# Performance work log

Hardware: AMD Instinct MI355X
Metric: run time of the kernel (lower is better)

The kernel has to match this reference:

```python
import jax, jax.numpy as jnp
import numpy as np

N_NEURONS = 1024
IN_NEURONS = 256
OUT_NEURONS = 128
ENERGY_SCALAR = 0.9


def setup_inputs() -> dict:
    key = jax.random.key(0)
    k1, k2 = jax.random.split(key)
    x = jax.random.normal(k1, (16384, IN_NEURONS), dtype=jnp.float32)
    # kaiming-uniform-like scale for an [n,n] fan_in=n matrix
    bound = float(np.sqrt(6.0 / N_NEURONS))
    weight = jax.random.uniform(k2, (N_NEURONS, N_NEURONS), dtype=jnp.float32,
                                minval=-bound, maxval=bound)
    return {"x": x, "weight": weight, "num_steps": 4}


def reference(x, weight, num_steps):
    # load_input_neurons: state[b,a,j] = s[b,a] * W[a,j], with s = pad(x) to n
    # We track m[b,a] such that state[b,a,j] = m[b,a]*W[a,j] at all times.
    N, D = x.shape
    n = weight.shape[0]
    m = jnp.pad(x, ((0, 0), (0, n - D)))  # [N, n]
    # step: colsum c[b,j] = sum_a m[b,a]*W[a,j] = m @ W; next state has m' = es * c
    for _ in range(num_steps):
        m = ENERGY_SCALAR * (m @ weight)
    # extract_output_neurons: Y[b,c] = state[b, -out+c, -out+c]
    diag_tail = jnp.diagonal(weight)[-OUT_NEURONS:]  # [out]
    y = m[:, -OUT_NEURONS:] * diag_tail  # [N, out]
    return y
```

## Files before the change

### kernel.cpp

```cpp
#include <hip/hip_runtime.h>
#include <stdint.h>

#define NW    1024
#define INW   256
#define OUTW  128
#define MROWS 16384
#define ES4   0.6561f

typedef __attribute__((ext_vector_type(8))) __bf16 bf16x8;
typedef __attribute__((ext_vector_type(4))) float f32x4;
typedef __attribute__((ext_vector_type(4))) unsigned short us4;

__device__ __forceinline__ unsigned short f2bf(float f) {
  uint32_t u = __builtin_bit_cast(uint32_t, f);
  u += 0x7fffu + ((u >> 16) & 1u);
  return (unsigned short)(u >> 16);
}

__device__ __forceinline__ void gload16(const void* g, void* lds) {
  __builtin_amdgcn_global_load_lds(
      (const __attribute__((address_space(1))) void*)g,
      (__attribute__((address_space(3))) void*)(uintptr_t)lds,
      16, 0, 0);
}

__device__ __forceinline__ int swz64(int a) { return a ^ (((a >> 6) & 3) << 4); }

__global__ void k_prep(const float* __restrict__ W, unsigned short* __restrict__ Wb,
                       unsigned short* __restrict__ Wt, float* __restrict__ sdiag) {
  __shared__ float t[32][33];
  const int tx = threadIdx.x & 31, ty = threadIdx.x >> 5;
  const int n0 = blockIdx.x * 32, k0 = blockIdx.y * 32;
#pragma unroll
  for (int j = 0; j < 4; ++j) {
    const int kk = ty * 4 + j;
    const float v = W[(size_t)(k0 + kk) * NW + n0 + tx];
    t[kk][tx] = v;
    Wb[(size_t)(k0 + kk) * NW + n0 + tx] = f2bf(v);
  }
  __syncthreads();
#pragma unroll
  for (int j = 0; j < 4; ++j) {
    const int nn = ty * 4 + j;
    Wt[(size_t)(n0 + nn) * NW + k0 + tx] = f2bf(t[tx][nn]);
  }
  if (n0 == k0 && n0 >= NW - OUTW && ty == 0)
    sdiag[n0 - (NW - OUTW) + tx] = ES4 * t[tx][tx];
}

__device__ __forceinline__ void g64x8(const unsigned short* __restrict__ A, int ldA,
                                      const unsigned short* __restrict__ Bt, int ldB,
                                      int K, char* ldsc,
                                      unsigned short* __restrict__ out, int ldOut,
                                      int mode, const float* __restrict__ sd)
{
  const int tid = threadIdx.x;
  const int grp = tid >> 8;
  const int t256 = tid & 255;
  const int wg = (tid >> 6) & 3;
  const int lane = tid & 63;
  const int wr = wg >> 1, wc = wg & 1;
  const int l15 = lane & 15, l4 = lane >> 4;
  const int kbase = grp * (K >> 1);
  const int nk = K >> 6;
  const int rb = grp * 32768;

  const int dst = t256 * 16;
  const int fa = swz64(dst);
  const int arow = fa >> 6, au = (fa >> 4) & 3;
  const unsigned short* gA = A + (size_t)arow * ldA + kbase + au * 8;
  const unsigned short* gB = Bt + (size_t)arow * ldB + kbase + au * 8;

  int idxA[2], idxB[2];
#pragma unroll
  for (int m = 0; m < 2; ++m)
    idxA[m] = rb + swz64(((wr * 32 + m * 16 + l15) * 4 + l4) * 16);
#pragma unroll
  for (int n = 0; n < 2; ++n)
    idxB[n] = rb + 16384 + swz64(((wc * 32 + n * 16 + l15) * 4 + l4) * 16);

  f32x4 acc[2][2];
#pragma unroll
  for (int m = 0; m < 2; ++m)
#pragma unroll
    for (int n = 0; n < 2; ++n) acc[m][n] = (f32x4){0.f, 0.f, 0.f, 0.f};

#pragma unroll
  for (int t = 0; t < 3; ++t) {
    const int sl = (t & 3) * 4096;
    gload16(gA + t * 32, ldsc + rb + sl + dst);
    gload16(gB + t * 32, ldsc + rb + 16384 + sl + dst);
  }
  asm volatile("s_waitcnt vmcnt(4)" ::: "memory");
  __builtin_amdgcn_s_barrier();

  for (int t = 0; t < nk; ++t) {
    const int bb = (t & 3) * 4096;
    const int sb = ((t + 3) & 3) * 4096;
    if (t + 3 < nk) {
      const int ko = (t + 3) * 32;
      gload16(gA + ko, ldsc + rb + sb + dst);
      gload16(gB + ko, ldsc + rb + 16384 + sb + dst);
    }
    bf16x8 af[2], bfr[2];
#pragma unroll
    for (int m = 0; m < 2; ++m) af[m] = *(const bf16x8*)(ldsc + bb + idxA[m]);
#pragma unroll
    for (int n = 0; n < 2; ++n) bfr[n] = *(const bf16x8*)(ldsc + bb + idxB[n]);
#pragma unroll
    for (int m = 0; m < 2; ++m)
#pragma unroll
      for (int n = 0; n < 2; ++n)
        acc[m][n] = __builtin_amdgcn_mfma_f32_16x16x32_bf16(af[m], bfr[n], acc[m][n], 0, 0, 0);
    if (t + 3 < nk)      asm volatile("s_waitcnt vmcnt(4)" ::: "memory");
    else if (t + 2 < nk) asm volatile("s_waitcnt vmcnt(2)" ::: "memory");
    else                 asm volatile("s_waitcnt vmcnt(0)" ::: "memory");
    __builtin_amdgcn_s_barrier();
  }

  if (grp == 0) {
    f32x4* wbase = (f32x4*)(ldsc + wg * 4096);
    wbase[lane * 4 + 0] = acc[0][0];
    wbase[lane * 4 + 1] = acc[0][1];
    wbase[lane * 4 + 2] = acc[1][0];
    wbase[lane * 4 + 3] = acc[1][1];
  }
  __builtin_amdgcn_s_barrier();
  if (grp == 1) {
    const f32x4* wbase = (const f32x4*)(ldsc + wg * 4096);
    acc[0][0] += wbase[lane * 4 + 0];
    acc[0][1] += wbase[lane * 4 + 1];
    acc[1][0] += wbase[lane * 4 + 2];
    acc[1][1] += wbase[lane * 4 + 3];
    if (mode == 0) {
#pragma unroll
      for (int m = 0; m < 2; ++m) {
        const int row0 = wr * 32 + m * 16 + l4 * 4;
#pragma unroll
        for (int n = 0; n < 2; ++n) {
          const int col = wc * 32 + n * 16 + l15;
#pragma unroll
          for (int r = 0; r < 4; ++r)
            out[(size_t)(row0 + r) * ldOut + col] = f2bf(acc[m][n][r]);
        }
      }
    } else {
#pragma unroll
      for (int m = 0; m < 2; ++m) {
        const int row0 = wr * 32 + m * 16 + l4 * 4;
#pragma unroll
        for (int n = 0; n < 2; ++n) {
          const int col = wc * 32 + n * 16 + l15;
          const float s = (mode == 2) ? sd[col] : 1.0f;
          us4 o = { f2bf(acc[m][n][0] * s), f2bf(acc[m][n][1] * s),
                    f2bf(acc[m][n][2] * s), f2bf(acc[m][n][3] * s) };
          *(us4*)&out[(size_t)col * ldOut + row0] = o;
        }
      }
    }
  }
}

__global__ __launch_bounds__(512, 1)
void kPQ(const unsigned short* __restrict__ Wb, const unsigned short* __restrict__ Wt,
         unsigned short* __restrict__ Pb, unsigned short* __restrict__ Qt)
{
  __shared__ __align__(16) char smem[65536];
  const int id = blockIdx.x;
  if (id < 64) {
    const int cx = id & 15, ry = id >> 4;
    g64x8(Wb + (size_t)ry * 64 * NW, NW, Wt + (size_t)cx * 64 * NW, NW, NW, smem,
          Pb + (size_t)ry * 64 * NW + cx * 64, NW, 0, nullptr);
  } else {
    const int q = id - 64;
    const int cx = q & 1, ry = q >> 1;
    g64x8(Wb + (size_t)ry * 64 * NW, NW,
          Wt + (size_t)(NW - OUTW + cx * 64) * NW, NW, NW, smem,
          Qt + (size_t)cx * 64 * NW + ry * 64, NW, 1, nullptr);
  }
}

__global__ __launch_bounds__(512, 1)
void kW4(const unsigned short* __restrict__ Pb, const unsigned short* __restrict__ Qt,
         const float* __restrict__ sdiag, unsigned short* __restrict__ W4s)
{
  __shared__ __align__(16) char smem[65536];
  const int cx = blockIdx.x & 1, ry = blockIdx.x >> 1;
  g64x8(Pb + (size_t)ry * 64 * NW, NW, Qt + (size_t)cx * 64 * NW, NW, NW, smem,
        W4s + (size_t)cx * 64 * INW + ry * 64, INW, 2, sdiag + cx * 64);
}

__global__ __launch_bounds__(64)
void k4(const float* __restrict__ x, const unsigned short* __restrict__ W4s,
        float* __restrict__ y)
{
  const int lane = threadIdx.x;
  const int l15 = lane & 15, l4 = lane >> 4;
  const int tRow = blockIdx.x * 16;

  const float* xrow = x + (size_t)(tRow + l15) * INW;
  float4 xa[8][2];
#pragma unroll
  for (int kk = 0; kk < 8; ++kk) {
    const int kb = l4 * 8 + kk * 32;
    xa[kk][0] = *(const float4*)(xrow + kb);
    xa[kk][1] = *(const float4*)(xrow + kb + 4);
  }

  f32x4 acc[8];
#pragma unroll
  for (int n = 0; n < 8; ++n) acc[n] = (f32x4){0.f, 0.f, 0.f, 0.f};

#pragma unroll
  for (int kk = 0; kk < 8; ++kk) {
    const int kb = l4 * 8 + kk * 32;
    bf16x8 af;
    af[0] = (__bf16)xa[kk][0].x; af[1] = (__bf16)xa[kk][0].y;
    af[2] = (__bf16)xa[kk][0].z; af[3] = (__bf16)xa[kk][0].w;
    af[4] = (__bf16)xa[kk][1].x; af[5] = (__bf16)xa[kk][1].y;
    af[6] = (__bf16)xa[kk][1].z; af[7] = (__bf16)xa[kk][1].w;
#pragma unroll
    for (int nf = 0; nf < 8; ++nf) {
      const bf16x8 bf = *(const bf16x8*)&W4s[(nf * 16 + l15) * 256 + kb];
      acc[nf] = __builtin_amdgcn_mfma_f32_16x16x32_bf16(af, bf, acc[nf], 0, 0, 0);
    }
  }

  const int row0 = tRow + l4 * 4;
#pragma unroll
  for (int nf = 0; nf < 8; ++nf)
#pragma unroll
    for (int r = 0; r < 4; ++r)
      y[(size_t)(row0 + r) * OUTW + nf * 16 + l15] = acc[nf][r];
}

extern "C" void kernel_launch(void* const* d_in, const int* in_sizes, int n_in,
                              void* d_out, int out_size, void* d_ws, size_t ws_size,
                              hipStream_t stream) {
  const float* x = (const float*)d_in[0];
  const float* W = (const float*)d_in[1];

  char* ws = (char*)d_ws;
  unsigned short* Wb   = (unsigned short*)(ws);
  unsigned short* Wt   = (unsigned short*)(ws + (2u << 20));
  unsigned short* Pb   = (unsigned short*)(ws + (4u << 20));
  unsigned short* Qt   = (unsigned short*)(ws + (5u << 20));
  unsigned short* W4s  = (unsigned short*)(ws + (6u << 20));
  float*          sdiag = (float*)(ws + (7u << 20));

  k_prep<<<dim3(NW / 32, NW / 32), 256, 0, stream>>>(W, Wb, Wt, sdiag);

  kPQ<<<dim3(96), 512, 0, stream>>>(Wb, Wt, Pb, Qt);

  kW4<<<dim3(8), 512, 0, stream>>>(Pb, Qt, sdiag, W4s);

  k4<<<dim3(MROWS / 16), 64, 0, stream>>>(x, W4s, (float*)d_out);
}
```

Baseline: 34.44 us.

## Fuse weight conversion into W² GEMM and read diagonal directly from W

Removes the k_prep kernel that converted W to bf16 and its transpose. The new kpq kernel loads fp32 W directly from global memory, converts it to bf16 in registers and feeds MFMA, with no LDS staging. kW4 now reads the scaled diagonal straight from W instead of a precomputed buffer. This saves one launch and a 4 MB bf16 round-trip. The cost is uncoalesced strided column loads for the B operand and no LDS reuse in the W@W GEMM.

```diff
diff --git a/kernel.cpp b/kernel.cpp
--- a/kernel.cpp
+++ b/kernel.cpp
@@ -10,6 +10,7 @@
 typedef __attribute__((ext_vector_type(8))) __bf16 bf16x8;
 typedef __attribute__((ext_vector_type(4))) float f32x4;
 typedef __attribute__((ext_vector_type(4))) unsigned short us4;
+typedef __attribute__((ext_vector_type(8))) unsigned short us8v;
 
 __device__ __forceinline__ unsigned short f2bf(float f) {
   uint32_t u = __builtin_bit_cast(uint32_t, f);
@@ -26,33 +27,88 @@
 
 __device__ __forceinline__ int swz64(int a) { return a ^ (((a >> 6) & 3) << 4); }
 
-__global__ void k_prep(const float* __restrict__ W, unsigned short* __restrict__ Wb,
-                       unsigned short* __restrict__ Wt, float* __restrict__ sdiag) {
-  __shared__ float t[32][33];
-  const int tx = threadIdx.x & 31, ty = threadIdx.x >> 5;
-  const int n0 = blockIdx.x * 32, k0 = blockIdx.y * 32;
-#pragma unroll
-  for (int j = 0; j < 4; ++j) {
-    const int kk = ty * 4 + j;
-    const float v = W[(size_t)(k0 + kk) * NW + n0 + tx];
-    t[kk][tx] = v;
-    Wb[(size_t)(k0 + kk) * NW + n0 + tx] = f2bf(v);
-  }
-  __syncthreads();
-#pragma unroll
-  for (int j = 0; j < 4; ++j) {
-    const int nn = ty * 4 + j;
-    Wt[(size_t)(n0 + nn) * NW + k0 + tx] = f2bf(t[tx][nn]);
-  }
-  if (n0 == k0 && n0 >= NW - OUTW && ty == 0)
-    sdiag[n0 - (NW - OUTW) + tx] = ES4 * t[tx][tx];
+__global__ __launch_bounds__(256)
+void kpq(const float* __restrict__ W, unsigned short* __restrict__ Pb,
+         unsigned short* __restrict__ Qt)
+{
+  const int b = blockIdx.x;
+  const int wv = threadIdx.x >> 6, lane = threadIdx.x & 63;
+  const int wr = wv >> 1, wc = wv & 1;
+  const int l15 = lane & 15, l4 = lane >> 4;
+
+  int r0, c0;
+  const bool isQ = (b >= 64);
+  if (!isQ) { r0 = (b >> 4) * 64; c0 = (b & 15) * 64; }
+  else      { const int q = b - 64; r0 = (q >> 1) * 64; c0 = 896 + (q & 1) * 64; }
+  const int wrow = r0 + wr * 32;
+  const int wcol = c0 + wc * 32;
+
+  f32x4 acc[2][2];
+#pragma unroll
+  for (int m = 0; m < 2; ++m)
+#pragma unroll
+    for (int n = 0; n < 2; ++n) acc[m][n] = (f32x4){0.f, 0.f, 0.f, 0.f};
+
+  for (int ks = 0; ks < 32; ++ks) {
+    const int kb = ks * 32 + l4 * 8;
+    bf16x8 af[2];
+#pragma unroll
+    for (int m = 0; m < 2; ++m) {
+      const float* ap = W + (size_t)(wrow + m * 16 + l15) * NW + kb;
+      const float4 a0 = *(const float4*)ap;
+      const float4 a1 = *(const float4*)(ap + 4);
+      us8v v = { f2bf(a0.x), f2bf(a0.y), f2bf(a0.z), f2bf(a0.w),
+                 f2bf(a1.x), f2bf(a1.y), f2bf(a1.z), f2bf(a1.w) };
+      af[m] = __builtin_bit_cast(bf16x8, v);
+    }
+    bf16x8 bfr[2];
+#pragma unroll
+    for (int n = 0; n < 2; ++n) {
+      const float* bp = W + (size_t)kb * NW + (wcol + n * 16 + l15);
+      us8v v = { f2bf(bp[0]),      f2bf(bp[NW]),     f2bf(bp[2 * NW]),
+                 f2bf(bp[3 * NW]), f2bf(bp[4 * NW]), f2bf(bp[5 * NW]),
+                 f2bf(bp[6 * NW]), f2bf(bp[7 * NW]) };
+      bfr[n] = __builtin_bit_cast(bf16x8, v);
+    }
+#pragma unroll
+    for (int m = 0; m < 2; ++m)
+#pragma unroll
+      for (int n = 0; n < 2; ++n)
+        acc[m][n] = __builtin_amdgcn_mfma_f32_16x16x32_bf16(af[m], bfr[n], acc[m][n], 0, 0, 0);
+  }
+
+  if (!isQ) {
+#pragma unroll
+    for (int m = 0; m < 2; ++m) {
+      const int row0 = wrow + m * 16 + l4 * 4;
+#pragma unroll
+      for (int n = 0; n < 2; ++n) {
+        const int col = wcol + n * 16 + l15;
+#pragma unroll
+        for (int r = 0; r < 4; ++r)
+          Pb[(size_t)(row0 + r) * NW + col] = f2bf(acc[m][n][r]);
+      }
+    }
+  } else {
+#pragma unroll
+    for (int m = 0; m < 2; ++m) {
+      const int row0 = wrow + m * 16 + l4 * 4;
+#pragma unroll
+      for (int n = 0; n < 2; ++n) {
+        const int col = wcol + n * 16 + l15;
+        us4 o = { f2bf(acc[m][n][0]), f2bf(acc[m][n][1]),
+                  f2bf(acc[m][n][2]), f2bf(acc[m][n][3]) };
+        *(us4*)&Qt[(size_t)(col - 896) * NW + row0] = o;
+      }
+    }
+  }
 }
 
 __device__ __forceinline__ void g64x8(const unsigned short* __restrict__ A, int ldA,
                                       const unsigned short* __restrict__ Bt, int ldB,
                                       int K, char* ldsc,
                                       unsigned short* __restrict__ out, int ldOut,
-                                      int mode, const float* __restrict__ sd)
+                                      const float* __restrict__ Wd)
 {
   const int tid = threadIdx.x;
   const int grp = tid >> 8;
@@ -132,62 +188,30 @@
     acc[0][1] += wbase[lane * 4 + 1];
     acc[1][0] += wbase[lane * 4 + 2];
     acc[1][1] += wbase[lane * 4 + 3];
-    if (mode == 0) {
-#pragma unroll
-      for (int m = 0; m < 2; ++m) {
-        const int row0 = wr * 32 + m * 16 + l4 * 4;
-#pragma unroll
-        for (int n = 0; n < 2; ++n) {
-          const int col = wc * 32 + n * 16 + l15;
-#pragma unroll
-          for (int r = 0; r < 4; ++r)
-            out[(size_t)(row0 + r) * ldOut + col] = f2bf(acc[m][n][r]);
-        }
+#pragma unroll
+    for (int m = 0; m < 2; ++m) {
+      const int row0 = wr * 32 + m * 16 + l4 * 4;
+#pragma unroll
+      for (int n = 0; n < 2; ++n) {
+        const int col = wc * 32 + n * 16 + l15;
+        const float s = ES4 * Wd[(size_t)col * (NW + 1)];
+        us4 o = { f2bf(acc[m][n][0] * s), f2bf(acc[m][n][1] * s),
+                  f2bf(acc[m][n][2] * s), f2bf(acc[m][n][3] * s) };
+        *(us4*)&out[(size_t)col * ldOut + row0] = o;
       }
-    } else {
-#pragma unroll
-      for (int m = 0; m < 2; ++m) {
-        const int row0 = wr * 32 + m * 16 + l4 * 4;
-#pragma unroll
-        for (int n = 0; n < 2; ++n) {
-          const int col = wc * 32 + n * 16 + l15;
-          const float s = (mode == 2) ? sd[col] : 1.0f;
-          us4 o = { f2bf(acc[m][n][0] * s), f2bf(acc[m][n][1] * s),
-                    f2bf(acc[m][n][2] * s), f2bf(acc[m][n][3] * s) };
-          *(us4*)&out[(size_t)col * ldOut + row0] = o;
-        }
-      }
-    }
-  }
-}
-
-__global__ __launch_bounds__(512, 1)
-void kPQ(const unsigned short* __restrict__ Wb, const unsigned short* __restrict__ Wt,
-         unsigned short* __restrict__ Pb, unsigned short* __restrict__ Qt)
-{
-  __shared__ __align__(16) char smem[65536];
-  const int id = blockIdx.x;
-  if (id < 64) {
-    const int cx = id & 15, ry = id >> 4;
-    g64x8(Wb + (size_t)ry * 64 * NW, NW, Wt + (size_t)cx * 64 * NW, NW, NW, smem,
-          Pb + (size_t)ry * 64 * NW + cx * 64, NW, 0, nullptr);
-  } else {
-    const int q = id - 64;
-    const int cx = q & 1, ry = q >> 1;
-    g64x8(Wb + (size_t)ry * 64 * NW, NW,
-          Wt + (size_t)(NW - OUTW + cx * 64) * NW, NW, NW, smem,
-          Qt + (size_t)cx * 64 * NW + ry * 64, NW, 1, nullptr);
+    }
   }
 }
 
 __global__ __launch_bounds__(512, 1)
 void kW4(const unsigned short* __restrict__ Pb, const unsigned short* __restrict__ Qt,
-         const float* __restrict__ sdiag, unsigned short* __restrict__ W4s)
+         const float* __restrict__ W, unsigned short* __restrict__ W4s)
 {
   __shared__ __align__(16) char smem[65536];
   const int cx = blockIdx.x & 1, ry = blockIdx.x >> 1;
+  const float* Wd = W + (size_t)(NW - OUTW + cx * 64) * (NW + 1);
   g64x8(Pb + (size_t)ry * 64 * NW, NW, Qt + (size_t)cx * 64 * NW, NW, NW, smem,
-        W4s + (size_t)cx * 64 * INW + ry * 64, INW, 2, sdiag + cx * 64);
+        W4s + (size_t)cx * 64 * INW + ry * 64, INW, Wd);
 }
 
 __global__ __launch_bounds__(64)
@@ -241,18 +265,13 @@
   const float* W = (const float*)d_in[1];
 
   char* ws = (char*)d_ws;
-  unsigned short* Wb   = (unsigned short*)(ws);
-  unsigned short* Wt   = (unsigned short*)(ws + (2u << 20));
-  unsigned short* Pb   = (unsigned short*)(ws + (4u << 20));
-  unsigned short* Qt   = (unsigned short*)(ws + (5u << 20));
-  unsigned short* W4s  = (unsigned short*)(ws + (6u << 20));
-  float*          sdiag = (float*)(ws + (7u << 20));
-
-  k_prep<<<dim3(NW / 32, NW / 32), 256, 0, stream>>>(W, Wb, Wt, sdiag);
-
-  kPQ<<<dim3(96), 512, 0, stream>>>(Wb, Wt, Pb, Qt);
-
-  kW4<<<dim3(8), 512, 0, stream>>>(Pb, Qt, sdiag, W4s);
+  unsigned short* Pb  = (unsigned short*)(ws);
+  unsigned short* Qt  = (unsigned short*)(ws + (1u << 20));
+  unsigned short* W4s = (unsigned short*)(ws + (2u << 20));
+
+  kpq<<<dim3(96), 256, 0, stream>>>(W, Pb, Qt);
+
+  kW4<<<dim3(8), 512, 0, stream>>>(Pb, Qt, W, W4s);
 
   k4<<<dim3(MROWS / 16), 64, 0, stream>>>(x, W4s, (float*)d_out);
 }
```

After: 53.48 us. 55.3% more time.
